# Kernel tuning notes

Measured on AMD Instinct MI355X. Metric: run time of the kernel, lower is better.

## Reference

```python
import jax, jax.numpy as jnp
import numpy as np

B, T, E, H, D = 4, 2048, 1024, 16, 64  # batch, seq (==context), embed, heads, head_size


def setup_inputs() -> dict:
    key = jax.random.key(0)
    ks = jax.random.split(key, 5)
    s_in = 1.0 / np.sqrt(E)
    s_c = 1.0 / np.sqrt(H * D)
    return {
        "x": jax.random.normal(ks[0], (B, T, E), dtype=jnp.float32),
        "Wq": jax.random.normal(ks[1], (H, E, D), dtype=jnp.float32) * s_in,
        "Wk": jax.random.normal(ks[2], (H, E, D), dtype=jnp.float32) * s_in,
        "Wv": jax.random.normal(ks[3], (H, E, D), dtype=jnp.float32) * s_in,
        "Wc": jax.random.normal(ks[4], (H * D, E), dtype=jnp.float32) * s_c,
    }


def reference(x, Wq, Wk, Wv, Wc):
    # Batched equivalent of the per-head Python loop: each head h does
    # q = x @ Wq[h], k = x @ Wk[h], v = x @ Wv[h]; causal softmax attention.
    q = jnp.einsum("bse,hed->bhsd", x, Wq)
    k = jnp.einsum("bte,hed->bhtd", x, Wk)
    v = jnp.einsum("bte,hed->bhtd", x, Wv)
    scale = 1.0 / jnp.sqrt(jnp.asarray(D, dtype=x.dtype))
    scores = jnp.einsum("bhsd,bhtd->bhst", q, k) * scale  # [B,H,T,T]
    causal = jnp.tril(jnp.ones((T, T), dtype=bool))
    scores = jnp.where(causal[None, None], scores, jnp.asarray(-jnp.inf, dtype=scores.dtype))
    attn = jax.nn.softmax(scores, axis=-1)
    out = jnp.einsum("bhst,bhtd->bhsd", attn, v)
    # concat heads along last dim (head 0 first), then combine linear
    out = out.transpose(0, 2, 1, 3).reshape(B, T, H * D)
    return out @ Wc
```

## Files before the change

kernel.cpp:

```cpp
#include <hip/hip_runtime.h>
#include <cstdint>
#include <cstddef>

typedef unsigned short u16;
typedef __bf16 bf16x8 __attribute__((ext_vector_type(8)));
typedef float f32x4 __attribute__((ext_vector_type(4)));
typedef float f32x16 __attribute__((ext_vector_type(16)));

#define B_ 4
#define T_ 2048
#define E_ 1024
#define H_ 16
#define D_ 64
#define HD3_ 3072
#define M_ (B_*T_)

__device__ __forceinline__ u16 f2bf(float f) {
  union { float f; unsigned u; } v; v.f = f;
  unsigned r = v.u + 0x7FFFu + ((v.u >> 16) & 1u);
  return (u16)(r >> 16);
}

__device__ __forceinline__ unsigned cvtpk(float a, float b) {
  unsigned r;
  asm("v_cvt_pk_bf16_f32 %0, %1, %2" : "=v"(r) : "v"(a), "v"(b));
  return r;
}

__device__ __forceinline__ void gl2lds16(const u16* g, u16* l) {
  __builtin_amdgcn_global_load_lds(
      (const __attribute__((address_space(1))) unsigned int*)g,
      (__attribute__((address_space(3))) unsigned int*)l, 16, 0, 0);
}

__global__ void prep_x(const float* __restrict__ x, u16* __restrict__ xb) {
  const long n4 = (long)(M_) * E_ / 4;
  for (long i = (long)blockIdx.x * blockDim.x + threadIdx.x; i < n4;
       i += (long)gridDim.x * blockDim.x) {
    float4 v = ((const float4*)x)[i];
    unsigned lo = (unsigned)f2bf(v.x) | ((unsigned)f2bf(v.y) << 16);
    unsigned hi = (unsigned)f2bf(v.z) | ((unsigned)f2bf(v.w) << 16);
    ((uint2*)xb)[i] = make_uint2(lo, hi);
  }
}

__global__ void prep_w(const float* __restrict__ Wq, const float* __restrict__ Wk,
                       const float* __restrict__ Wv, const float* __restrict__ Wc,
                       u16* __restrict__ WT, u16* __restrict__ WcT) {
  const int total = HD3_ * E_ + E_ * E_;
  for (int i = blockIdx.x * blockDim.x + threadIdx.x; i < total;
       i += gridDim.x * blockDim.x) {
    if (i < HD3_ * E_) {
      int n = i >> 10, e = i & 1023;
      int mtx = n >> 10, hd = n & 1023, h = hd >> 6, d = hd & 63;
      const float* W = (mtx == 0) ? Wq : (mtx == 1) ? Wk : Wv;
      WT[i] = f2bf(W[((size_t)h * E_ + e) * D_ + d]);
    } else {
      int j = i - HD3_ * E_;
      int n = j >> 10, k = j & 1023;
      WcT[j] = f2bf(Wc[(size_t)k * E_ + n]);
    }
  }
}

template<int N_, bool OUT_BF16>
__global__ __launch_bounds__(512, 2) void gemm8(
    const u16* __restrict__ A, const u16* __restrict__ Bt,
    void* __restrict__ Cv, float qscale)
{
  __shared__ u16 As[2][128 * 64];
  __shared__ u16 Bs[2][256 * 64];
  const int tid = threadIdx.x;
  const int lane = tid & 63, w = tid >> 6;
  const int wr = w >> 2, wc = w & 3;
  const int l15 = lane & 15, l4 = lane >> 4;

  const int gx = N_ / 256;
  const int lin = blockIdx.x;
  const int cpx = (gx * 64) >> 3;
  const int swz = (lin & 7) * cpx + (lin >> 3);
  const int bxi = swz % gx, byi = swz / gx;
  const size_t bm = (size_t)byi * 128, bn = (size_t)bxi * 256;
  const u16* Ag = A + bm * 1024;
  const u16* Bg = Bt + bn * 1024;

  auto stageA = [&](int b, int t, int i) {
    int idx = i * 512 + tid, r = idx >> 3, c = idx & 7;
    gl2lds16(Ag + (size_t)r * 1024 + t * 64 + ((c ^ (r & 7)) * 8), &As[b][idx * 8]);
  };
  auto stageB = [&](int b, int t, int i) {
    int idx = i * 512 + tid, r = idx >> 3, c = idx & 7;
    gl2lds16(Bg + (size_t)r * 1024 + t * 64 + ((c ^ (r & 7)) * 8), &Bs[b][idx * 8]);
  };

  int aoff[4][2], boff[4][2];
#pragma unroll
  for (int m = 0; m < 4; ++m) {
    int r = wr * 64 + m * 16 + l15;
#pragma unroll
    for (int s = 0; s < 2; ++s)
      aoff[m][s] = r * 64 + (((s * 4 + l4) ^ (r & 7)) * 8);
  }
#pragma unroll
  for (int n = 0; n < 4; ++n) {
    int r = wc * 64 + n * 16 + l15;
#pragma unroll
    for (int s = 0; s < 2; ++s)
      boff[n][s] = r * 64 + (((s * 4 + l4) ^ (r & 7)) * 8);
  }

  f32x4 acc[4][4] = {};

#pragma unroll
  for (int i = 0; i < 2; ++i) stageA(0, 0, i);
#pragma unroll
  for (int i = 0; i < 4; ++i) stageB(0, 0, i);
#pragma unroll
  for (int i = 0; i < 2; ++i) stageA(1, 1, i);
  asm volatile("s_waitcnt vmcnt(2)" ::: "memory");
  __builtin_amdgcn_s_barrier();

  for (int t = 0; t < 16; ++t) {
    const int cur = t & 1;
    bf16x8 af[4][2], bfv[4][2];
#pragma unroll
    for (int m = 0; m < 4; ++m)
#pragma unroll
      for (int s = 0; s < 2; ++s)
        af[m][s] = *(const bf16x8*)&As[cur][aoff[m][s]];
#pragma unroll
    for (int n = 0; n < 2; ++n)
#pragma unroll
      for (int s = 0; s < 2; ++s)
        bfv[n][s] = *(const bf16x8*)&Bs[cur][boff[n][s]];
    if (t + 1 < 16) {
      stageB(cur ^ 1, t + 1, 0);
      stageB(cur ^ 1, t + 1, 1);
      stageB(cur ^ 1, t + 1, 2);
    }
    __builtin_amdgcn_s_barrier();
    asm volatile("s_waitcnt lgkmcnt(0)" ::: "memory");
    __builtin_amdgcn_sched_barrier(0);
    __builtin_amdgcn_s_setprio(1);
#pragma unroll
    for (int m = 0; m < 4; ++m)
#pragma unroll
      for (int n = 0; n < 2; ++n)
#pragma unroll
        for (int s = 0; s < 2; ++s)
          acc[m][n] = __builtin_amdgcn_mfma_f32_16x16x32_bf16(
              af[m][s], bfv[n][s], acc[m][n], 0, 0, 0);
    __builtin_amdgcn_s_setprio(0);
    __builtin_amdgcn_s_barrier();

#pragma unroll
    for (int n = 2; n < 4; ++n)
#pragma unroll
      for (int s = 0; s < 2; ++s)
        bfv[n][s] = *(const bf16x8*)&Bs[cur][boff[n][s]];
    if (t + 1 < 16) stageB(cur ^ 1, t + 1, 3);
    if (t + 2 < 16) { stageA(cur, t + 2, 0); stageA(cur, t + 2, 1); }
    __builtin_amdgcn_s_barrier();
    asm volatile("s_waitcnt lgkmcnt(0)" ::: "memory");
    __builtin_amdgcn_sched_barrier(0);
    __builtin_amdgcn_s_setprio(1);
#pragma unroll
    for (int m = 0; m < 4; ++m)
#pragma unroll
      for (int n = 2; n < 4; ++n)
#pragma unroll
        for (int s = 0; s < 2; ++s)
          acc[m][n] = __builtin_amdgcn_mfma_f32_16x16x32_bf16(
              af[m][s], bfv[n][s], acc[m][n], 0, 0, 0);
    __builtin_amdgcn_s_setprio(0);
    if (t + 2 < 16)      asm volatile("s_waitcnt vmcnt(2)" ::: "memory");
    else if (t + 1 < 16) asm volatile("s_waitcnt vmcnt(0)" ::: "memory");
    __builtin_amdgcn_s_barrier();
  }

#pragma unroll
  for (int m = 0; m < 4; ++m)
#pragma unroll
    for (int n = 0; n < 4; ++n) {
      size_t row = bm + wr * 64 + m * 16 + l4 * 4;
      size_t col = bn + wc * 64 + n * 16 + l15;
      float sc = (col < 1024) ? qscale : 1.0f;
#pragma unroll
      for (int j = 0; j < 4; ++j) {
        if (OUT_BF16)
          ((u16*)Cv)[(row + j) * N_ + col] = f2bf(acc[m][n][j] * sc);
        else
          ((float*)Cv)[(row + j) * N_ + col] = acc[m][n][j];
      }
    }
}

__global__ __launch_bounds__(256) void transpose_v(const u16* __restrict__ QKV,
                                                   u16* __restrict__ VT) {
  const int bh = blockIdx.y, b = bh >> 4, h = bh & 15;
  const int t0 = blockIdx.x * 64;
  __shared__ u16 tile[64][72];
  const int tid = threadIdx.x;
  const u16* src = QKV + ((size_t)(b * T_ + t0) * HD3_ + 2048 + h * 64);
#pragma unroll
  for (int i = 0; i < 2; ++i) {
    int c = i * 256 + tid;
    int r = c >> 3, cc = (c & 7) * 8;
    uint4 v = *(const uint4*)(src + (size_t)r * HD3_ + cc);
    *(uint4*)&tile[r][cc] = v;
  }
  __syncthreads();
  u16* dst = VT + (size_t)bh * D_ * T_ + t0;
#pragma unroll
  for (int i = 0; i < 16; ++i) {
    int idx = i * 256 + tid;
    int d = idx >> 6, tl = idx & 63;
    dst[(size_t)d * T_ + tl] = tile[tl][d];
  }
}

__global__ __launch_bounds__(256, 2) void attn_kernel(
    const u16* __restrict__ QKV, const u16* __restrict__ VT,
    u16* __restrict__ O)
{
  __shared__ u16 Ks[2][4096];
  __shared__ u16 Vs[2][4096];
  const int L = blockIdx.x;
  const int bh = L & 63, b = bh >> 4, h = bh & 15;
  const int qt = 15 - (L >> 6);
  const int q0 = qt * 128;
  const int tid = threadIdx.x, w = tid >> 6, lane = tid & 63;
  const int ql = lane & 31, hi = lane >> 5;
  const int qw0 = q0 + w * 32;

  const u16* Qg = QKV + ((size_t)(b * T_ + q0) * HD3_ + h * 64);
  const u16* Kg = QKV + ((size_t)(b * T_) * HD3_ + 1024 + h * 64);
  const u16* Vg = VT + (size_t)bh * (D_ * T_);

#pragma unroll
  for (int i = 0; i < 4; ++i) {
    int c = i * 256 + tid, r = c >> 3, cc = c & 7, sc = cc ^ (r & 7);
    gl2lds16(Qg + (size_t)r * HD3_ + sc * 8, &Ks[0][0] + c * 8);
  }
  __syncthreads();
  bf16x8 qf[4];
  {
    int qrow = w * 32 + ql;
#pragma unroll
    for (int s = 0; s < 4; ++s) {
      int ch = (2 * s + hi) ^ (qrow & 7);
      qf[s] = *(const bf16x8*)(&Ks[0][0] + qrow * 64 + ch * 8);
    }
  }
  __syncthreads();

#pragma unroll
  for (int i = 0; i < 2; ++i) {
    int c = i * 256 + tid, r = c >> 3, cc = c & 7, sc = cc ^ (r & 7);
    gl2lds16(Kg + (size_t)r * HD3_ + sc * 8, &Ks[0][0] + c * 8);
    gl2lds16(Vg + (size_t)r * T_ + sc * 8, &Vs[0][0] + c * 8);
  }

  f32x16 acc[2];
#pragma unroll
  for (int ni = 0; ni < 2; ++ni)
#pragma unroll
    for (int r = 0; r < 16; ++r) acc[ni][r] = 0.f;
  float mrun = -1e30f, lrun = 0.f;
  const int ktmax = 2 * qt + 2;

  for (int kt = 0; kt < ktmax; ++kt) {
    const int cur = kt & 1;
    const int kv0 = kt * 64;
    __syncthreads();
    if (kt + 1 < ktmax) {
      const int nkv = kv0 + 64;
#pragma unroll
      for (int i = 0; i < 2; ++i) {
        int c = i * 256 + tid, r = c >> 3, cc = c & 7, sc = cc ^ (r & 7);
        gl2lds16(Kg + (size_t)(nkv + r) * HD3_ + sc * 8, &Ks[cur ^ 1][0] + c * 8);
        gl2lds16(Vg + (size_t)r * T_ + nkv + sc * 8, &Vs[cur ^ 1][0] + c * 8);
      }
    }
    if (kv0 > qw0 + 31) continue;

    f32x16 st[2];
#pragma unroll
    for (int f = 0; f < 2; ++f)
#pragma unroll
      for (int r = 0; r < 16; ++r) st[f][r] = 0.f;
    __builtin_amdgcn_s_setprio(1);
#pragma unroll
    for (int f = 0; f < 2; ++f) {
      const int krow = f * 32 + ql;
      const int swzr = krow & 7;
#pragma unroll
      for (int s = 0; s < 4; ++s) {
        int ch = (2 * s + hi) ^ swzr;
        bf16x8 kfr = *(const bf16x8*)(&Ks[cur][0] + krow * 64 + ch * 8);
        st[f] = __builtin_amdgcn_mfma_f32_32x32x16_bf16(kfr, qf[s], st[f], 0, 0, 0);
      }
    }
    __builtin_amdgcn_s_setprio(0);

    if (kv0 + 63 > qw0) {
      const int qg = qw0 + ql;
#pragma unroll
      for (int f = 0; f < 2; ++f)
#pragma unroll
        for (int r = 0; r < 16; ++r) {
          int kg = kv0 + f * 32 + (r & 3) + 8 * (r >> 2) + 4 * hi;
          if (kg > qg) st[f][r] = -1e30f;
        }
    }

    float mt = st[0][0];
#pragma unroll
    for (int f = 0; f < 2; ++f)
#pragma unroll
      for (int r = 0; r < 16; ++r) mt = fmaxf(mt, st[f][r]);
    mt = fmaxf(mt, __shfl_xor(mt, 32, 64));
    if (!__all(mt - mrun <= 8.f)) {
      float mnew = fmaxf(mrun, mt);
      float corr = exp2f(mrun - mnew);
      lrun *= corr;
#pragma unroll
      for (int ni = 0; ni < 2; ++ni)
#pragma unroll
        for (int r = 0; r < 16; ++r) acc[ni][r] *= corr;
      mrun = mnew;
    }
    float sum = 0.f;
#pragma unroll
    for (int f = 0; f < 2; ++f)
#pragma unroll
      for (int r = 0; r < 16; ++r) {
        float p = exp2f(st[f][r] - mrun);
        st[f][r] = p;
        sum += p;
      }
    sum += __shfl_xor(sum, 32, 64);
    lrun += sum;

    __builtin_amdgcn_s_setprio(1);
#pragma unroll
    for (int s = 0; s < 4; ++s) {
      const int f = s >> 1, bse = (s & 1) * 8;
      unsigned b0 = cvtpk(st[f][bse + 0], st[f][bse + 1]);
      unsigned b1 = cvtpk(st[f][bse + 2], st[f][bse + 3]);
      unsigned a0 = cvtpk(st[f][bse + 4], st[f][bse + 5]);
      unsigned a1 = cvtpk(st[f][bse + 6], st[f][bse + 7]);
      asm volatile("v_permlane32_swap_b32 %0, %1" : "+v"(b0), "+v"(a0));
      asm volatile("v_permlane32_swap_b32 %0, %1" : "+v"(b1), "+v"(a1));
      union { unsigned u[4]; bf16x8 v; } pa;
      pa.u[0] = b0; pa.u[1] = b1; pa.u[2] = a0; pa.u[3] = a1;
#pragma unroll
      for (int ni = 0; ni < 2; ++ni) {
        int vrow = ni * 32 + ql;
        int ch = (2 * s + hi) ^ (vrow & 7);
        bf16x8 vf = *(const bf16x8*)(&Vs[cur][0] + vrow * 64 + ch * 8);
        acc[ni] = __builtin_amdgcn_mfma_f32_32x32x16_bf16(vf, pa.v, acc[ni], 0, 0, 0);
      }
    }
    __builtin_amdgcn_s_setprio(0);
  }

  const int q = q0 + w * 32 + ql;
  u16* Og = O + ((size_t)(b * T_ + q) * (H_ * D_) + h * 64);
  const float inv = 1.f / lrun;
#pragma unroll
  for (int ni = 0; ni < 2; ++ni)
#pragma unroll
    for (int rr = 0; rr < 8; ++rr) {
      const int r0 = rr * 2;
      const int d0 = ((r0 & 3) + 8 * (r0 >> 2)) + 4 * hi + ni * 32;
      unsigned pk = cvtpk(acc[ni][r0] * inv, acc[ni][r0 + 1] * inv);
      *(unsigned*)(Og + d0) = pk;
    }
}

extern "C" void kernel_launch(void* const* d_in, const int* in_sizes, int n_in,
                              void* d_out, int out_size, void* d_ws, size_t ws_size,
                              hipStream_t stream) {
  const float* x  = (const float*)d_in[0];
  const float* Wq = (const float*)d_in[1];
  const float* Wk = (const float*)d_in[2];
  const float* Wv = (const float*)d_in[3];
  const float* Wc = (const float*)d_in[4];

  char* ws = (char*)d_ws;
  u16* xb  = (u16*)(ws);
  u16* WT  = (u16*)(ws + 16777216);
  u16* WcT = (u16*)(ws + 23068672);
  u16* QKV = (u16*)(ws + 25165824);
  u16* Ob  = (u16*)(ws + 75497472);
  u16* VT  = xb;
  float* out = (float*)d_out;

  const float QSCALE = 0.125f * 1.4426950408889634f;

  prep_x<<<2048, 256, 0, stream>>>(x, xb);
  prep_w<<<4096, 256, 0, stream>>>(Wq, Wk, Wv, Wc, WT, WcT);
  gemm8<3072, true><<<768, 512, 0, stream>>>(xb, WT, QKV, QSCALE);
  transpose_v<<<dim3(32, 64), 256, 0, stream>>>(QKV, VT);
  attn_kernel<<<dim3(1024), 256, 0, stream>>>(QKV, VT, Ob);
  gemm8<1024, false><<<256, 512, 0, stream>>>(Ob, WcT, out, 1.0f);
}
```

Measured before the change: 266.8 us.

## Tune attention kernel occupancy, tile ordering, and softmax arithmetic

```diff
diff --git a/kernel.cpp b/kernel.cpp
--- a/kernel.cpp
+++ b/kernel.cpp
@@ -14,6 +14,17 @@
 #define D_ 64
 #define HD3_ 3072
 #define M_ (B_*T_)
+
+#if __has_builtin(__builtin_amdgcn_exp2f)
+#define EXP2F(x) __builtin_amdgcn_exp2f(x)
+#else
+#define EXP2F(x) exp2f(x)
+#endif
+#if __has_builtin(__builtin_amdgcn_rcpf)
+#define RCPF(x) __builtin_amdgcn_rcpf(x)
+#else
+#define RCPF(x) (1.f/(x))
+#endif
 
 __device__ __forceinline__ u16 f2bf(float f) {
   union { float f; unsigned u; } v; v.f = f;
@@ -219,7 +230,7 @@
   }
 }
 
-__global__ __launch_bounds__(256, 2) void attn_kernel(
+__global__ __launch_bounds__(256, 4) void attn_kernel(
     const u16* __restrict__ QKV, const u16* __restrict__ VT,
     u16* __restrict__ O)
 {
@@ -227,7 +238,8 @@
   __shared__ u16 Vs[2][4096];
   const int L = blockIdx.x;
   const int bh = L & 63, b = bh >> 4, h = bh & 15;
-  const int qt = 15 - (L >> 6);
+  const int jj = L >> 8, gg = (L >> 6) & 3;
+  const int qt = 4 * jj + ((gg + jj) & 3);
   const int q0 = qt * 128;
   const int tid = threadIdx.x, w = tid >> 6, lane = tid & 63;
   const int ql = lane & 31, hi = lane >> 5;
@@ -254,12 +266,30 @@
   }
   __syncthreads();
 
-#pragma unroll
-  for (int i = 0; i < 2; ++i) {
-    int c = i * 256 + tid, r = c >> 3, cc = c & 7, sc = cc ^ (r & 7);
-    gl2lds16(Kg + (size_t)r * HD3_ + sc * 8, &Ks[0][0] + c * 8);
-    gl2lds16(Vg + (size_t)r * T_ + sc * 8, &Vs[0][0] + c * 8);
-  }
+  int koff[2][4];
+#pragma unroll
+  for (int f = 0; f < 2; ++f) {
+    int row = f * 32 + ql, swzr = row & 7;
+#pragma unroll
+    for (int s = 0; s < 4; ++s)
+      koff[f][s] = row * 64 + (((2 * s + hi) ^ swzr) * 8);
+  }
+
+  const int c0 = tid, c1 = 256 + tid;
+  const int r0_ = c0 >> 3, sc0 = (c0 & 7) ^ (r0_ & 7);
+  const int r1_ = c1 >> 3, sc1 = (c1 & 7) ^ (r1_ & 7);
+  const int lo0 = c0 * 8, lo1 = c1 * 8;
+  const u16* kp0 = Kg + (size_t)r0_ * HD3_ + sc0 * 8;
+  const u16* kp1 = Kg + (size_t)r1_ * HD3_ + sc1 * 8;
+  const u16* vp0 = Vg + (size_t)r0_ * T_ + sc0 * 8;
+  const u16* vp1 = Vg + (size_t)r1_ * T_ + sc1 * 8;
+
+  gl2lds16(kp0, &Ks[0][lo0]);
+  gl2lds16(kp1, &Ks[0][lo1]);
+  gl2lds16(vp0, &Vs[0][lo0]);
+  gl2lds16(vp1, &Vs[0][lo1]);
+  kp0 += 64 * HD3_; kp1 += 64 * HD3_;
+  vp0 += 64; vp1 += 64;
 
   f32x16 acc[2];
 #pragma unroll
@@ -274,15 +304,18 @@
     const int kv0 = kt * 64;
     __syncthreads();
     if (kt + 1 < ktmax) {
-      const int nkv = kv0 + 64;
-#pragma unroll
-      for (int i = 0; i < 2; ++i) {
-        int c = i * 256 + tid, r = c >> 3, cc = c & 7, sc = cc ^ (r & 7);
-        gl2lds16(Kg + (size_t)(nkv + r) * HD3_ + sc * 8, &Ks[cur ^ 1][0] + c * 8);
-        gl2lds16(Vg + (size_t)r * T_ + nkv + sc * 8, &Vs[cur ^ 1][0] + c * 8);
-      }
+      u16* kb = &Ks[cur ^ 1][0];
+      u16* vb = &Vs[cur ^ 1][0];
+      gl2lds16(kp0, kb + lo0);
+      gl2lds16(kp1, kb + lo1);
+      gl2lds16(vp0, vb + lo0);
+      gl2lds16(vp1, vb + lo1);
+      kp0 += 64 * HD3_; kp1 += 64 * HD3_;
+      vp0 += 64; vp1 += 64;
     }
     if (kv0 > qw0 + 31) continue;
+    const u16* kbase = &Ks[cur][0];
+    const u16* vbase = &Vs[cur][0];
 
     f32x16 st[2];
 #pragma unroll
@@ -291,16 +324,12 @@
       for (int r = 0; r < 16; ++r) st[f][r] = 0.f;
     __builtin_amdgcn_s_setprio(1);
 #pragma unroll
-    for (int f = 0; f < 2; ++f) {
-      const int krow = f * 32 + ql;
-      const int swzr = krow & 7;
+    for (int f = 0; f < 2; ++f)
 #pragma unroll
       for (int s = 0; s < 4; ++s) {
-        int ch = (2 * s + hi) ^ swzr;
-        bf16x8 kfr = *(const bf16x8*)(&Ks[cur][0] + krow * 64 + ch * 8);
+        bf16x8 kfr = *(const bf16x8*)(kbase + koff[f][s]);
         st[f] = __builtin_amdgcn_mfma_f32_32x32x16_bf16(kfr, qf[s], st[f], 0, 0, 0);
       }
-    }
     __builtin_amdgcn_s_setprio(0);
 
     if (kv0 + 63 > qw0) {
@@ -314,15 +343,18 @@
         }
     }
 
-    float mt = st[0][0];
-#pragma unroll
-    for (int f = 0; f < 2; ++f)
-#pragma unroll
-      for (int r = 0; r < 16; ++r) mt = fmaxf(mt, st[f][r]);
-    mt = fmaxf(mt, __shfl_xor(mt, 32, 64));
+    float tr[16];
+#pragma unroll
+    for (int r = 0; r < 16; ++r) tr[r] = fmaxf(st[0][r], st[1][r]);
+#pragma unroll
+    for (int ss = 8; ss; ss >>= 1)
+#pragma unroll
+      for (int r = 0; r < 8; ++r)
+        if (r < ss) tr[r] = fmaxf(tr[r], tr[r + ss]);
+    float mt = fmaxf(tr[0], __shfl_xor(tr[0], 32, 64));
     if (!__all(mt - mrun <= 8.f)) {
       float mnew = fmaxf(mrun, mt);
-      float corr = exp2f(mrun - mnew);
+      float corr = EXP2F(mrun - mnew);
       lrun *= corr;
 #pragma unroll
       for (int ni = 0; ni < 2; ++ni)
@@ -330,17 +362,19 @@
         for (int r = 0; r < 16; ++r) acc[ni][r] *= corr;
       mrun = mnew;
     }
-    float sum = 0.f;
+
 #pragma unroll
     for (int f = 0; f < 2; ++f)
 #pragma unroll
-      for (int r = 0; r < 16; ++r) {
-        float p = exp2f(st[f][r] - mrun);
-        st[f][r] = p;
-        sum += p;
-      }
-    sum += __shfl_xor(sum, 32, 64);
-    lrun += sum;
+      for (int r = 0; r < 16; ++r) st[f][r] = EXP2F(st[f][r] - mrun);
+#pragma unroll
+    for (int r = 0; r < 16; ++r) tr[r] = st[0][r] + st[1][r];
+#pragma unroll
+    for (int ss = 8; ss; ss >>= 1)
+#pragma unroll
+      for (int r = 0; r < 8; ++r)
+        if (r < ss) tr[r] += tr[r + ss];
+    lrun += tr[0] + __shfl_xor(tr[0], 32, 64);
 
     __builtin_amdgcn_s_setprio(1);
 #pragma unroll
@@ -356,9 +390,7 @@
       pa.u[0] = b0; pa.u[1] = b1; pa.u[2] = a0; pa.u[3] = a1;
 #pragma unroll
       for (int ni = 0; ni < 2; ++ni) {
-        int vrow = ni * 32 + ql;
-        int ch = (2 * s + hi) ^ (vrow & 7);
-        bf16x8 vf = *(const bf16x8*)(&Vs[cur][0] + vrow * 64 + ch * 8);
+        bf16x8 vf = *(const bf16x8*)(vbase + koff[ni][s]);
         acc[ni] = __builtin_amdgcn_mfma_f32_32x32x16_bf16(vf, pa.v, acc[ni], 0, 0, 0);
       }
     }
@@ -367,7 +399,7 @@
 
   const int q = q0 + w * 32 + ql;
   u16* Og = O + ((size_t)(b * T_ + q) * (H_ * D_) + h * 64);
-  const float inv = 1.f / lrun;
+  const float inv = RCPF(lrun);
 #pragma unroll
   for (int ni = 0; ni < 2; ++ni)
 #pragma unroll
```

After: 260.2 us. 2.5% less time.
